# Kernel optimization log

Measured on AMD Instinct MI355X. Metric: run time of the kernel, lower is better.

## Reference

```python
import jax, jax.numpy as jnp
import numpy as np
import math

B, S = 2, 2048
D_IN = 512
D_OUT = 512
P = 8
K = 8


def setup_inputs() -> dict:
    key = jax.random.key(0)
    ks = jax.random.split(key, 8)
    mean_phi = math.log(math.sqrt(2.0 / (D_IN * K)))
    mean_w2 = math.log(math.sqrt(2.0 / D_OUT))
    x = jax.random.normal(ks[0], (B, S, D_IN), dtype=jnp.float32)
    phi_raw = mean_phi + 0.2 * jax.random.normal(ks[1], (D_OUT, D_IN * K), dtype=jnp.float32)
    phi_bias = jnp.zeros((D_OUT,), dtype=jnp.float32)
    raw_weight2 = mean_w2 + 0.2 * jax.random.normal(ks[2], (P, D_OUT, D_OUT), dtype=jnp.float32)
    bias2 = jnp.zeros((P, D_OUT), dtype=jnp.float32)
    gate_raw2 = jnp.full((P,), -3.0, dtype=jnp.float32)
    # kaiming_uniform with a=sqrt(5) on shape (P, 2*D_in, D_out): fan_in = 2*D_in
    bound = math.sqrt(6.0 / ((1.0 + 5.0) * (2 * D_IN)))
    z_weight = jax.random.uniform(ks[3], (P, 2 * D_IN, D_OUT), dtype=jnp.float32,
                                  minval=-bound, maxval=bound)
    gate_raw = jnp.full((P,), -3.0, dtype=jnp.float32)
    output_bias = jnp.zeros((P, D_OUT), dtype=jnp.float32)
    return {
        "x": x, "phi_raw": phi_raw, "phi_bias": phi_bias,
        "raw_weight2": raw_weight2, "bias2": bias2, "gate_raw2": gate_raw2,
        "z_weight": z_weight, "gate_raw": gate_raw, "output_bias": output_bias,
    }


def reference(x, phi_raw, phi_bias, raw_weight2, bias2, gate_raw2,
              z_weight, gate_raw, output_bias):
    sp = jax.nn.softplus
    orig = x.shape
    x_flat = x.reshape(-1, D_IN)                              # [N, Din]
    N = x_flat.shape[0]
    shifts = jnp.linspace(-1.0, 1.0, K, dtype=x.dtype)        # [k]
    phi = sp(x_flat[:, :, None] + shifts[None, None, :])      # [N, Din, k]
    phi_flat = phi.reshape(N, D_IN * K)                       # [N, Din*k]
    # PositiveLinearHK: weight = softplus(raw)^2
    w_phi = jnp.square(sp(phi_raw))                           # [Dout, Din*k]
    x_proj = phi_flat @ w_phi.T + phi_bias                    # [N, Dout]
    g1 = jax.nn.sigmoid(gate_raw)[:, None, None]              # [P,1,1]
    z0 = sp(x_proj[None, :, :] * g1)                          # [P, N, Dout]
    w2 = jnp.square(sp(raw_weight2))                          # [P, Dout, Dout]
    # bmm(z0, w2.transpose(1,2)) == einsum over the second Dout axis of w2
    z1 = jnp.einsum('pnd,ped->pne', z0, w2) + bias2[:, None, :]
    g2 = jax.nn.sigmoid(gate_raw2)[:, None, None]
    z1 = sp(z1 * g2)                                          # [P, N, Dout]
    x_res_in = jnp.concatenate([x_flat, x_flat], axis=-1)     # [N, 2*Din]
    x_res = jnp.einsum('nc,pce->pne', x_res_in, z_weight)     # [P, N, Dout]
    z_final = sp(z1 + x_res) + output_bias[:, None, :]        # [P, N, Dout]
    out = jnp.transpose(z_final, (1, 0, 2))                   # [N, P, Dout]
    return out.reshape(tuple(orig[:-1]) + (P, D_OUT))
```

## Files before the change

### kernel.cpp

```cpp
#include <hip/hip_runtime.h>

typedef unsigned short u16;
typedef __attribute__((ext_vector_type(8))) short bf16x8;
typedef __attribute__((ext_vector_type(4))) float floatx4;
typedef __attribute__((ext_vector_type(8))) unsigned short u16x8;
typedef __attribute__((ext_vector_type(4))) unsigned short u16x4;

#define NTOK 4096
#define DDIN 512
#define DDOUT 512
#define NP 8

__device__ __forceinline__ float b2f(u16 b) {
    union { unsigned int u; float f; } v; v.u = ((unsigned int)b) << 16; return v.f;
}
__device__ __forceinline__ u16 f2b(float f) {
    union { float f; unsigned int u; } v; v.f = f;
    unsigned int r = (v.u + 0x7fffu + ((v.u >> 16) & 1u)) >> 16;
    return (u16)r;
}
__device__ __forceinline__ float sp(float x) {
    return fmaxf(x, 0.f) + __logf(1.f + __expf(-fabsf(x)));
}
__device__ __forceinline__ float sigm(float x) { return 1.f / (1.f + __expf(-x)); }

__device__ __forceinline__ void gld16(const u16* g, u16* l) {
    __builtin_amdgcn_global_load_lds((const __attribute__((address_space(1))) void*)g,
                                     (__attribute__((address_space(3))) void*)l, 16, 0, 0);
}

__global__ void prep_sqsp2(const float* __restrict__ in1, u16* __restrict__ out1, int n1,
                           const float* __restrict__ in2, u16* __restrict__ out2, int n2) {
    int i = blockIdx.x * 256 + threadIdx.x;
    if (i < n1) {
        float s = sp(in1[i]);
        out1[i] = f2b(s * s);
    } else if (i - n1 < n2) {
        int j = i - n1;
        float s = sp(in2[j]);
        out2[j] = f2b(s * s);
    }
}

__global__ void prep_zwT(const float* __restrict__ zw, u16* __restrict__ zwT) {
    int p = blockIdx.z;
    int c0 = blockIdx.x * 32, e0 = blockIdx.y * 32;
    __shared__ float tb[32][33];
    int tx = threadIdx.x, ty = threadIdx.y;
    const float* base = zw + (size_t)p * 1024 * 512;
#pragma unroll
    for (int r = 0; r < 4; ++r) {
        int cl = ty * 4 + r;
        float a = base[(size_t)(c0 + cl) * 512 + e0 + tx];
        float b = base[(size_t)(c0 + cl + 512) * 512 + e0 + tx];
        tb[cl][tx] = a + b;
    }
    __syncthreads();
    u16* outb = zwT + (size_t)p * 512 * 512;
#pragma unroll
    for (int r = 0; r < 4; ++r) {
        int el = ty * 4 + r;
        outb[(size_t)(e0 + el) * 512 + c0 + tx] = f2b(tb[tx][el]);
    }
}

__global__ void phi_kernel(const float* __restrict__ x, u16* __restrict__ phi,
                           u16* __restrict__ xb) {
    int i = blockIdx.x * 256 + threadIdx.x;
    float xv = x[i];
    xb[i] = f2b(xv);
    u16x8 v;
#pragma unroll
    for (int k = 0; k < 8; ++k) {
        float s = -1.f + (2.f / 7.f) * (float)k;
        v[k] = f2b(sp(xv + s));
    }
    *(u16x8*)(phi + (size_t)i * 8) = v;
}


__launch_bounds__(256, 3)
__global__ void gemm1p(const u16* __restrict__ phi, const u16* __restrict__ wphi,
                       u16* __restrict__ xpart) {
    __shared__ __align__(16) u16 lds[2 * 8192];
    u16* As = lds;
    u16* Bs = lds + 8192;

    const int id = blockIdx.x;
    const int kc = id & 7;
    const int local = id >> 3;
    const int o0 = (local & 3) * 128;
    const int n0 = (local >> 2) * 128;
    const int kbase = kc * 512;

    const int t = threadIdx.x;
    const int wave = t >> 6, lane = t & 63;
    const int wm = wave >> 1, wn = wave & 1;
    const int l15 = lane & 15, quad = lane >> 4;
    const int srow = t >> 3;
    const int sgx = (((t & 7) ^ (srow & 7))) * 8;

    floatx4 acc[4][4];
#pragma unroll
    for (int i = 0; i < 4; ++i)
#pragma unroll
        for (int j = 0; j < 4; ++j) acc[i][j] = {0.f, 0.f, 0.f, 0.f};

    for (int k0 = 0; k0 < 512; k0 += 64) {
        const u16* ga = phi + (size_t)(n0 + srow) * 4096 + kbase + k0 + sgx;
        const u16* gb = wphi + (size_t)(o0 + srow) * 4096 + kbase + k0 + sgx;
        __syncthreads();
#pragma unroll
        for (int c = 0; c < 4; ++c) {
            gld16(ga + (size_t)c * 32 * 4096, As + c * 2048 + t * 8);
            gld16(gb + (size_t)c * 32 * 4096, Bs + c * 2048 + t * 8);
        }
        __syncthreads();
#pragma unroll
        for (int ks = 0; ks < 2; ++ks) {
            bf16x8 a[4], b[4];
#pragma unroll
            for (int s = 0; s < 4; ++s) {
                int ra = wm * 64 + s * 16 + l15;
                int rb = wn * 64 + s * 16 + l15;
                a[s] = *(const bf16x8*)(As + ra * 64 + (((ks * 4 + quad) ^ (ra & 7)) * 8));
                b[s] = *(const bf16x8*)(Bs + rb * 64 + (((ks * 4 + quad) ^ (rb & 7)) * 8));
            }
#pragma unroll
            for (int sm = 0; sm < 4; ++sm)
#pragma unroll
                for (int sn = 0; sn < 4; ++sn)
                    acc[sm][sn] = __builtin_amdgcn_mfma_f32_16x16x32_bf16(a[sm], b[sn], acc[sm][sn], 0, 0, 0);
        }
    }

    u16* xp = xpart + (size_t)kc * NTOK * DDOUT;
#pragma unroll
    for (int sm = 0; sm < 4; ++sm)
#pragma unroll
        for (int sn = 0; sn < 4; ++sn) {
            int gcol = o0 + wn * 64 + sn * 16 + l15;
#pragma unroll
            for (int r = 0; r < 4; ++r) {
                int grow = n0 + wm * 64 + sm * 16 + quad * 4 + r;
                xp[(size_t)grow * DDOUT + gcol] = f2b(acc[sm][sn][r]);
            }
        }
}

__global__ void reduce_ep(const u16* __restrict__ xpart, const float* __restrict__ phi_bias,
                          const float* __restrict__ gate_raw, u16* __restrict__ z0) {
    int idx = blockIdx.x * 256 + threadIdx.x;
    int n = idx >> 7;
    int o4 = (idx & 127) * 4;
    size_t base = (size_t)n * DDOUT + o4;
    float s0 = 0.f, s1 = 0.f, s2 = 0.f, s3 = 0.f;
#pragma unroll
    for (int kc = 0; kc < 8; ++kc) {
        u16x4 v = *(const u16x4*)(xpart + (size_t)kc * NTOK * DDOUT + base);
        s0 += b2f(v[0]); s1 += b2f(v[1]); s2 += b2f(v[2]); s3 += b2f(v[3]);
    }
    floatx4 pb = *(const floatx4*)(phi_bias + o4);
    s0 += pb[0]; s1 += pb[1]; s2 += pb[2]; s3 += pb[3];
#pragma unroll
    for (int p = 0; p < NP; ++p) {
        float g = sigm(gate_raw[p]);
        u16x4 v;
        v[0] = f2b(sp(s0 * g)); v[1] = f2b(sp(s1 * g));
        v[2] = f2b(sp(s2 * g)); v[3] = f2b(sp(s3 * g));
        *(u16x4*)(z0 + (size_t)p * NTOK * DDOUT + base) = v;
    }
}

__launch_bounds__(256, 2)
__global__ void gemm23(const u16* __restrict__ z0, const u16* __restrict__ w2b,
                       const u16* __restrict__ xb, const u16* __restrict__ zwT,
                       const float* __restrict__ bias2, const float* __restrict__ gate_raw2,
                       const float* __restrict__ output_bias, float* __restrict__ out) {
    __shared__ __align__(16) u16 lds[4 * 8192];
    u16* A1 = lds;
    u16* B1 = lds + 8192;
    u16* A2 = lds + 16384;
    u16* B2 = lds + 24576;

    const int id = blockIdx.x;
    const int p = id & 7;
    const int local = id >> 3;
    const int e0 = (local & 3) * 128;
    const int n0 = (local >> 2) * 128;

    const int t = threadIdx.x;
    const int wave = t >> 6, lane = t & 63;
    const int wm = wave >> 1, wn = wave & 1;
    const int l15 = lane & 15, quad = lane >> 4;
    const int srow = t >> 3;
    const int sgx = (((t & 7) ^ (srow & 7))) * 8;

    const u16* z0p = z0 + (size_t)p * NTOK * DDOUT;
    const u16* w2p = w2b + (size_t)p * DDOUT * DDOUT;
    const u16* zwp = zwT + (size_t)p * DDOUT * DDIN;

    floatx4 acc1[4][4], acc2[4][4];
#pragma unroll
    for (int i = 0; i < 4; ++i)
#pragma unroll
        for (int j = 0; j < 4; ++j) {
            acc1[i][j] = {0.f, 0.f, 0.f, 0.f};
            acc2[i][j] = {0.f, 0.f, 0.f, 0.f};
        }

    for (int k0 = 0; k0 < 512; k0 += 64) {
        const u16* ga1 = z0p + (size_t)(n0 + srow) * 512 + k0 + sgx;
        const u16* gb1 = w2p + (size_t)(e0 + srow) * 512 + k0 + sgx;
        const u16* ga2 = xb  + (size_t)(n0 + srow) * 512 + k0 + sgx;
        const u16* gb2 = zwp + (size_t)(e0 + srow) * 512 + k0 + sgx;
        __syncthreads();
#pragma unroll
        for (int c = 0; c < 4; ++c) {
            gld16(ga1 + (size_t)c * 32 * 512, A1 + c * 2048 + t * 8);
            gld16(gb1 + (size_t)c * 32 * 512, B1 + c * 2048 + t * 8);
            gld16(ga2 + (size_t)c * 32 * 512, A2 + c * 2048 + t * 8);
            gld16(gb2 + (size_t)c * 32 * 512, B2 + c * 2048 + t * 8);
        }
        __syncthreads();
#pragma unroll
        for (int ks = 0; ks < 2; ++ks) {
            bf16x8 a1[4], b1[4], a2[4], b2[4];
#pragma unroll
            for (int s = 0; s < 4; ++s) {
                int ra = wm * 64 + s * 16 + l15;
                int rb = wn * 64 + s * 16 + l15;
                int ko = ((ks * 4 + quad) ^ (ra & 7)) * 8;
                a1[s] = *(const bf16x8*)(A1 + ra * 64 + ko);
                b1[s] = *(const bf16x8*)(B1 + rb * 64 + ko);
                a2[s] = *(const bf16x8*)(A2 + ra * 64 + ko);
                b2[s] = *(const bf16x8*)(B2 + rb * 64 + ko);
            }
#pragma unroll
            for (int sm = 0; sm < 4; ++sm)
#pragma unroll
                for (int sn = 0; sn < 4; ++sn) {
                    acc1[sm][sn] = __builtin_amdgcn_mfma_f32_16x16x32_bf16(a1[sm], b1[sn], acc1[sm][sn], 0, 0, 0);
                    acc2[sm][sn] = __builtin_amdgcn_mfma_f32_16x16x32_bf16(a2[sm], b2[sn], acc2[sm][sn], 0, 0, 0);
                }
        }
    }

    const float g2p = sigm(gate_raw2[p]);
#pragma unroll
    for (int sm = 0; sm < 4; ++sm)
#pragma unroll
        for (int sn = 0; sn < 4; ++sn) {
            int gcol = e0 + wn * 64 + sn * 16 + l15;
            float bb = bias2[p * DDOUT + gcol];
            float ob = output_bias[p * DDOUT + gcol];
#pragma unroll
            for (int r = 0; r < 4; ++r) {
                int grow = n0 + wm * 64 + sm * 16 + quad * 4 + r;
                float v1 = acc1[sm][sn][r] + bb;
                float o = sp(sp(v1 * g2p) + acc2[sm][sn][r]) + ob;
                out[(size_t)grow * (NP * DDOUT) + p * DDOUT + gcol] = o;
            }
        }
}

extern "C" void kernel_launch(void* const* d_in, const int* in_sizes, int n_in,
                              void* d_out, int out_size, void* d_ws, size_t ws_size,
                              hipStream_t stream) {
    const float* x           = (const float*)d_in[0];
    const float* phi_raw     = (const float*)d_in[1];
    const float* phi_bias    = (const float*)d_in[2];
    const float* raw_weight2 = (const float*)d_in[3];
    const float* bias2       = (const float*)d_in[4];
    const float* gate_raw2   = (const float*)d_in[5];
    const float* z_weight    = (const float*)d_in[6];
    const float* gate_raw    = (const float*)d_in[7];
    const float* output_bias = (const float*)d_in[8];
    float* out = (float*)d_out;

    u16* ws   = (u16*)d_ws;
    u16* phi  = ws;
    u16* wphi = phi + (size_t)4096 * 4096;
    u16* w2b  = wphi + (size_t)512 * 4096;
    u16* zwT  = w2b + (size_t)8 * 512 * 512;
    u16* z0   = zwT + (size_t)8 * 512 * 512;
    u16* xb   = z0 + (size_t)8 * 4096 * 512;
    u16* xpart = (u16*)d_out;

    const int n1 = 512 * 4096, n2 = 8 * 512 * 512;
    hipLaunchKernelGGL(prep_sqsp2, dim3((n1 + n2) / 256), dim3(256), 0, stream,
                       phi_raw, wphi, n1, raw_weight2, w2b, n2);
    hipLaunchKernelGGL(prep_zwT, dim3(16, 16, 8), dim3(32, 8), 0, stream, z_weight, zwT);
    hipLaunchKernelGGL(phi_kernel, dim3(8192), dim3(256), 0, stream, x, phi, xb);
    hipLaunchKernelGGL(gemm1p, dim3(1024), dim3(256), 0, stream, phi, wphi, xpart);
    hipLaunchKernelGGL(reduce_ep, dim3(2048), dim3(256), 0, stream, xpart, phi_bias, gate_raw, z0);
    hipLaunchKernelGGL(gemm23, dim3(1024), dim3(256), 0, stream,
                       z0, w2b, xb, zwT, bias2, gate_raw2, output_bias, out);
}
```

Measured before the change: 209.2 us.

## Merge prep kernels and fuse split-K reduction into gemm1 via last-block counter

Combines the three preprocessing kernels into one launch with block-range dispatch, and vectorises the weight softplus-square pass. The separate split-K reduce/epilogue kernel is removed: each gemm1 tile increments an atomic counter, and the last of the eight K-chunk blocks sums the partials and writes z0 for all gates. This aims to cut launch overhead and one full pass over the partial buffer, at the cost of a serialized tail on the last-arriving blocks and dependence on fence/atomic ordering.

```diff
diff --git a/kernel.cpp b/kernel.cpp
--- a/kernel.cpp
+++ b/kernel.cpp
@@ -29,62 +29,74 @@
                                      (__attribute__((address_space(3))) void*)l, 16, 0, 0);
 }
 
-__global__ void prep_sqsp2(const float* __restrict__ in1, u16* __restrict__ out1, int n1,
-                           const float* __restrict__ in2, u16* __restrict__ out2, int n2) {
-    int i = blockIdx.x * 256 + threadIdx.x;
-    if (i < n1) {
-        float s = sp(in1[i]);
-        out1[i] = f2b(s * s);
-    } else if (i - n1 < n2) {
-        int j = i - n1;
-        float s = sp(in2[j]);
-        out2[j] = f2b(s * s);
+__global__ void prep_all(const float* __restrict__ x, u16* __restrict__ phi,
+                         u16* __restrict__ xb,
+                         const float* __restrict__ phi_raw, u16* __restrict__ wphi,
+                         const float* __restrict__ raw_weight2, u16* __restrict__ w2b,
+                         const float* __restrict__ zw, u16* __restrict__ zwT,
+                         unsigned* __restrict__ cnt) {
+    __shared__ float tb[32][33];
+    const int bid = blockIdx.x, t = threadIdx.x;
+    if (bid < 8192) {
+        int i = bid * 256 + t;
+        float xv = x[i];
+        xb[i] = f2b(xv);
+        u16x8 v;
+#pragma unroll
+        for (int k = 0; k < 8; ++k) {
+            float s = -1.f + (2.f / 7.f) * (float)k;
+            v[k] = f2b(sp(xv + s));
+        }
+        *(u16x8*)(phi + (size_t)i * 8) = v;
+    } else if (bid < 12288) {
+        const int n1 = 512 * 4096;
+        int i = (bid - 8192) * 1024 + t * 4;
+        const float* src = (i < n1) ? phi_raw + i : raw_weight2 + (i - n1);
+        u16* dst = (i < n1) ? wphi + i : w2b + (i - n1);
+        floatx4 vv = *(const floatx4*)src;
+        u16x4 o;
+#pragma unroll
+        for (int j = 0; j < 4; ++j) {
+            float s = sp(vv[j]);
+            o[j] = f2b(s * s);
+        }
+        *(u16x4*)dst = o;
+    } else if (bid < 14336) {
+        int idx = bid - 12288;
+        int p = idx >> 8;
+        int rem = idx & 255;
+        int c0 = (rem & 15) * 32, e0 = (rem >> 4) * 32;
+        int tx = t & 31, ty = t >> 5;
+        const float* base = zw + (size_t)p * 1024 * 512;
+#pragma unroll
+        for (int r = 0; r < 4; ++r) {
+            int cl = ty * 4 + r;
+            float a = base[(size_t)(c0 + cl) * 512 + e0 + tx];
+            float b = base[(size_t)(c0 + cl + 512) * 512 + e0 + tx];
+            tb[cl][tx] = a + b;
+        }
+        __syncthreads();
+        u16* outb = zwT + (size_t)p * 512 * 512;
+#pragma unroll
+        for (int r = 0; r < 4; ++r) {
+            int el = ty * 4 + r;
+            outb[(size_t)(e0 + el) * 512 + c0 + tx] = f2b(tb[tx][el]);
+        }
+    } else {
+        if (t < 128) cnt[t] = 0u;
     }
 }
 
-__global__ void prep_zwT(const float* __restrict__ zw, u16* __restrict__ zwT) {
-    int p = blockIdx.z;
-    int c0 = blockIdx.x * 32, e0 = blockIdx.y * 32;
-    __shared__ float tb[32][33];
-    int tx = threadIdx.x, ty = threadIdx.y;
-    const float* base = zw + (size_t)p * 1024 * 512;
-#pragma unroll
-    for (int r = 0; r < 4; ++r) {
-        int cl = ty * 4 + r;
-        float a = base[(size_t)(c0 + cl) * 512 + e0 + tx];
-        float b = base[(size_t)(c0 + cl + 512) * 512 + e0 + tx];
-        tb[cl][tx] = a + b;
-    }
-    __syncthreads();
-    u16* outb = zwT + (size_t)p * 512 * 512;
-#pragma unroll
-    for (int r = 0; r < 4; ++r) {
-        int el = ty * 4 + r;
-        outb[(size_t)(e0 + el) * 512 + c0 + tx] = f2b(tb[tx][el]);
-    }
-}
-
-__global__ void phi_kernel(const float* __restrict__ x, u16* __restrict__ phi,
-                           u16* __restrict__ xb) {
-    int i = blockIdx.x * 256 + threadIdx.x;
-    float xv = x[i];
-    xb[i] = f2b(xv);
-    u16x8 v;
-#pragma unroll
-    for (int k = 0; k < 8; ++k) {
-        float s = -1.f + (2.f / 7.f) * (float)k;
-        v[k] = f2b(sp(xv + s));
-    }
-    *(u16x8*)(phi + (size_t)i * 8) = v;
-}
-
-
 __launch_bounds__(256, 3)
-__global__ void gemm1p(const u16* __restrict__ phi, const u16* __restrict__ wphi,
-                       u16* __restrict__ xpart) {
+__global__ void gemm1pz(const u16* __restrict__ phi, const u16* __restrict__ wphi,
+                        u16* __restrict__ xpart,
+                        const float* __restrict__ phi_bias,
+                        const float* __restrict__ gate_raw,
+                        u16* __restrict__ z0, unsigned* __restrict__ cnt) {
     __shared__ __align__(16) u16 lds[2 * 8192];
     u16* As = lds;
     u16* Bs = lds + 8192;
+    __shared__ int amLast;
 
     const int id = blockIdx.x;
     const int kc = id & 7;
@@ -146,29 +158,39 @@
                 xp[(size_t)grow * DDOUT + gcol] = f2b(acc[sm][sn][r]);
             }
         }
-}
-
-__global__ void reduce_ep(const u16* __restrict__ xpart, const float* __restrict__ phi_bias,
-                          const float* __restrict__ gate_raw, u16* __restrict__ z0) {
-    int idx = blockIdx.x * 256 + threadIdx.x;
-    int n = idx >> 7;
-    int o4 = (idx & 127) * 4;
-    size_t base = (size_t)n * DDOUT + o4;
-    float s0 = 0.f, s1 = 0.f, s2 = 0.f, s3 = 0.f;
-#pragma unroll
-    for (int kc = 0; kc < 8; ++kc) {
-        u16x4 v = *(const u16x4*)(xpart + (size_t)kc * NTOK * DDOUT + base);
-        s0 += b2f(v[0]); s1 += b2f(v[1]); s2 += b2f(v[2]); s3 += b2f(v[3]);
-    }
-    floatx4 pb = *(const floatx4*)(phi_bias + o4);
-    s0 += pb[0]; s1 += pb[1]; s2 += pb[2]; s3 += pb[3];
-#pragma unroll
-    for (int p = 0; p < NP; ++p) {
-        float g = sigm(gate_raw[p]);
-        u16x4 v;
-        v[0] = f2b(sp(s0 * g)); v[1] = f2b(sp(s1 * g));
-        v[2] = f2b(sp(s2 * g)); v[3] = f2b(sp(s3 * g));
-        *(u16x4*)(z0 + (size_t)p * NTOK * DDOUT + base) = v;
+
+    __threadfence();
+    __syncthreads();
+    if (t == 0) amLast = (atomicAdd(&cnt[local], 1u) == 7u) ? 1 : 0;
+    __syncthreads();
+    if (!amLast) return;
+    __threadfence();
+
+    float g1[NP];
+#pragma unroll
+    for (int p = 0; p < NP; ++p) g1[p] = sigm(gate_raw[p]);
+
+    for (int g = 0; g < 16; ++g) {
+        int idx = g * 256 + t;
+        int r = idx >> 5;
+        int cg = (idx & 31) * 4;
+        size_t base = (size_t)(n0 + r) * DDOUT + o0 + cg;
+        float s0 = 0.f, s1 = 0.f, s2 = 0.f, s3 = 0.f;
+#pragma unroll
+        for (int kk = 0; kk < 8; ++kk) {
+            u16x4 v = *(const u16x4*)(xpart + (size_t)kk * NTOK * DDOUT + base);
+            s0 += b2f(v[0]); s1 += b2f(v[1]); s2 += b2f(v[2]); s3 += b2f(v[3]);
+        }
+        floatx4 pb = *(const floatx4*)(phi_bias + o0 + cg);
+        s0 += pb[0]; s1 += pb[1]; s2 += pb[2]; s3 += pb[3];
+#pragma unroll
+        for (int p = 0; p < NP; ++p) {
+            float gg = g1[p];
+            u16x4 v;
+            v[0] = f2b(sp(s0 * gg)); v[1] = f2b(sp(s1 * gg));
+            v[2] = f2b(sp(s2 * gg)); v[3] = f2b(sp(s3 * gg));
+            *(u16x4*)(z0 + (size_t)p * NTOK * DDOUT + base) = v;
+        }
     }
 }
 
@@ -285,15 +307,14 @@
     u16* zwT  = w2b + (size_t)8 * 512 * 512;
     u16* z0   = zwT + (size_t)8 * 512 * 512;
     u16* xb   = z0 + (size_t)8 * 4096 * 512;
+
     u16* xpart = (u16*)d_out;
-
-    const int n1 = 512 * 4096, n2 = 8 * 512 * 512;
-    hipLaunchKernelGGL(prep_sqsp2, dim3((n1 + n2) / 256), dim3(256), 0, stream,
-                       phi_raw, wphi, n1, raw_weight2, w2b, n2);
-    hipLaunchKernelGGL(prep_zwT, dim3(16, 16, 8), dim3(32, 8), 0, stream, z_weight, zwT);
-    hipLaunchKernelGGL(phi_kernel, dim3(8192), dim3(256), 0, stream, x, phi, xb);
-    hipLaunchKernelGGL(gemm1p, dim3(1024), dim3(256), 0, stream, phi, wphi, xpart);
-    hipLaunchKernelGGL(reduce_ep, dim3(2048), dim3(256), 0, stream, xpart, phi_bias, gate_raw, z0);
+    unsigned* cnt = (unsigned*)((char*)d_out + 48u * 1024u * 1024u);
+
+    hipLaunchKernelGGL(prep_all, dim3(14337), dim3(256), 0, stream,
+                       x, phi, xb, phi_raw, wphi, raw_weight2, w2b, z_weight, zwT, cnt);
+    hipLaunchKernelGGL(gemm1pz, dim3(1024), dim3(256), 0, stream,
+                       phi, wphi, xpart, phi_bias, gate_raw, z0, cnt);
     hipLaunchKernelGGL(gemm23, dim3(1024), dim3(256), 0, stream,
                        z0, w2b, xb, zwT, bias2, gate_raw2, output_bias, out);
 }
```

Measured after the change: 477.4 us. 128% more time.
